# Kernel tuning notes

Hardware: AMD Instinct MI355X
Metric: run time of the kernel (lower is better)

## Reference

```python
import jax, jax.numpy as jnp
import numpy as np

B, S1, S2 = 16, 256, 512          # batch, vision len, text len
V_HID, T_HID = 1024, 768          # v_hidden_size, hidden_size
BI_HID, H = 1024, 8               # bi_hidden_size, bi_num_attention_heads
D = BI_HID // H                   # attention_head_size = 128


def setup_inputs() -> dict:
    key = jax.random.key(0)
    ks = jax.random.split(key, 16)
    s = 0.02
    inp = {
        "input_tensor1": jax.random.normal(ks[0], (B, S1, V_HID), jnp.float32),
        "attention_mask1": jnp.zeros((B, 1, 1, S1), jnp.float32),
        "input_tensor2": jax.random.normal(ks[1], (B, S2, T_HID), jnp.float32),
        "attention_mask2": jnp.zeros((B, 1, 1, S2), jnp.float32),
        # vision-stream projections (query1/key1/value1): v_hidden -> all_head_size
        "Wq1": jax.random.normal(ks[2], (V_HID, BI_HID), jnp.float32) * s,
        "bq1": jnp.zeros((BI_HID,), jnp.float32),
        "Wk1": jax.random.normal(ks[3], (V_HID, BI_HID), jnp.float32) * s,
        "bk1": jnp.zeros((BI_HID,), jnp.float32),
        "Wv1": jax.random.normal(ks[4], (V_HID, BI_HID), jnp.float32) * s,
        "bv1": jnp.zeros((BI_HID,), jnp.float32),
        # text-stream projections (query2/key2/value2): hidden -> all_head_size
        "Wq2": jax.random.normal(ks[5], (T_HID, BI_HID), jnp.float32) * s,
        "bq2": jnp.zeros((BI_HID,), jnp.float32),
        "Wk2": jax.random.normal(ks[6], (T_HID, BI_HID), jnp.float32) * s,
        "bk2": jnp.zeros((BI_HID,), jnp.float32),
        "Wv2": jax.random.normal(ks[7], (T_HID, BI_HID), jnp.float32) * s,
        "bv2": jnp.zeros((BI_HID,), jnp.float32),
    }
    return inp


def _heads(x):
    # [B, S, H*D] -> [B, S, H, D]
    b, s, _ = x.shape
    return x.reshape(b, s, H, D)


def reference(input_tensor1, attention_mask1, input_tensor2, attention_mask2,
              Wq1, bq1, Wk1, bk1, Wv1, bv1,
              Wq2, bq2, Wk2, bk2, Wv2, bv2):
    scale = 1.0 / jnp.sqrt(jnp.asarray(D, input_tensor1.dtype))
    # stream 1 (vision) QKV
    q1 = _heads(input_tensor1 @ Wq1 + bq1)
    k1 = _heads(input_tensor1 @ Wk1 + bk1)
    v1 = _heads(input_tensor1 @ Wv1 + bv1)
    # stream 2 (text) QKV
    q2 = _heads(input_tensor2 @ Wq2 + bq2)
    k2 = _heads(input_tensor2 @ Wk2 + bk2)
    v2 = _heads(input_tensor2 @ Wv2 + bv2)

    # attention 1: text queries attend to vision keys/values  -> context1 [B,S2,BI_HID]
    scores1 = jnp.einsum('bqhd,bkhd->bhqk', q2, k1) * scale + attention_mask1
    probs1 = jax.nn.softmax(scores1, axis=-1)  # dropout prob = 0 (eval)
    context1 = jnp.einsum('bhqk,bkhd->bqhd', probs1, v1).reshape(B, S2, BI_HID)

    # attention 2: vision queries attend to text keys/values  -> context2 [B,S1,BI_HID]
    scores2 = jnp.einsum('bqhd,bkhd->bhqk', q1, k2) * scale + attention_mask2
    probs2 = jax.nn.softmax(scores2, axis=-1)
    context2 = jnp.einsum('bhqk,bkhd->bqhd', probs2, v2).reshape(B, S1, BI_HID)

    return (context1, context2)
```

## Files before the change

### kernel.cpp

```cpp
#include <hip/hip_runtime.h>


typedef _Float16 f16;
typedef unsigned int u32;
typedef f16  v8h __attribute__((ext_vector_type(8)));
typedef float v4f __attribute__((ext_vector_type(4)));

struct alignas(8) h4 { f16 x, y, z, w; };

#define GLL16(g, l) __builtin_amdgcn_global_load_lds(                          \
    (const __attribute__((address_space(1))) u32*)(g),                         \
    (__attribute__((address_space(3))) u32*)(l), 16, 0, 0)

#define MFMA16 __builtin_amdgcn_mfma_f32_16x16x32_f16

__global__ __launch_bounds__(256)
void cvt_in(const float* __restrict__ p1, long n1,
            const float* __restrict__ p2, long n2,
            f16* __restrict__ d1, f16* __restrict__ d2)
{
    long i = ((long)blockIdx.x * 256 + threadIdx.x) * 8;
    const float* s; f16* d;
    if (i < n1) { s = p1 + i; d = d1 + i; }
    else        { long j = i - n1; if (j >= n2) return; s = p2 + j; d = d2 + j; }
    float4 a = *(const float4*)s, b = *(const float4*)(s + 4);
    v8h o = {(f16)a.x, (f16)a.y, (f16)a.z, (f16)a.w,
             (f16)b.x, (f16)b.y, (f16)b.z, (f16)b.w};
    *(v8h*)d = o;
}

__global__ __launch_bounds__(256)
void cvt_wT(const float* __restrict__ w0, const float* __restrict__ w1,
            const float* __restrict__ w2, const float* __restrict__ w3,
            const float* __restrict__ w4, const float* __restrict__ w5,
            f16* __restrict__ o1, f16* __restrict__ o2)
{
    const int z = blockIdx.z;
    const int K = z < 3 ? 1024 : 768;
    const int bk = blockIdx.y * 64;
    if (bk >= K) return;
    const float* src = z == 0 ? w0 : z == 1 ? w1 : z == 2 ? w2
                     : z == 3 ? w3 : z == 4 ? w4 : w5;
    f16* dst = z < 3 ? o1 + (size_t)z * 1024 * 1024
                     : o2 + (size_t)(z - 3) * 1024 * 768;

    __shared__ float t[64][65];
    const int bn = blockIdx.x * 64;
    const int r0 = threadIdx.x >> 4, c4 = (threadIdx.x & 15) * 4;
#pragma unroll
    for (int rr = 0; rr < 64; rr += 16) {
        float4 v = *(const float4*)&src[(long)(bk + rr + r0) * 1024 + bn + c4];
        t[rr + r0][c4 + 0] = v.x; t[rr + r0][c4 + 1] = v.y;
        t[rr + r0][c4 + 2] = v.z; t[rr + r0][c4 + 3] = v.w;
    }
    __syncthreads();
#pragma unroll
    for (int rr = 0; rr < 64; rr += 16) {
        const int n = rr + r0;
        h4 o = {(f16)t[c4 + 0][n], (f16)t[c4 + 1][n],
                (f16)t[c4 + 2][n], (f16)t[c4 + 3][n]};
        *(h4*)&dst[(long)(bn + n) * K + bk + c4] = o;
    }
}

__global__ __launch_bounds__(256, 4)
void mm_proj(const f16* __restrict__ A2, const f16* __restrict__ B2,
             const float* __restrict__ bq2, const float* __restrict__ bk2,
             const float* __restrict__ bv2,
             f16* __restrict__ q2o, f16* __restrict__ k2o, f16* __restrict__ v2o,
             const f16* __restrict__ A1, const f16* __restrict__ B1,
             const float* __restrict__ bq1, const float* __restrict__ bk1,
             const float* __restrict__ bv1,
             f16* __restrict__ q1o, f16* __restrict__ k1o, f16* __restrict__ v1o)
{
    __shared__ f16 sh[16384];

    const int gid = blockIdx.x;
    const bool is2 = gid < 1536;
    const int id   = is2 ? gid : gid - 1536;
    const int K    = is2 ? 768 : 1024;
    const int S    = is2 ? 512 : 256;
    const int mdiv = is2 ? 8 : 4;
    const f16* A  = is2 ? A2 : A1;
    const f16* Bw = is2 ? B2 : B1;

    const int by = (id & 7) * mdiv + ((id >> 3) % mdiv);
    const int bx = id / (8 * mdiv);
    const int m0 = by * 128, n0 = bx * 128;

    const int tid = threadIdx.x, lane = tid & 63, w = tid >> 6;
    const int wm = w >> 1, wn = w & 1;
    const int fr = lane & 15, fq = lane >> 4;

    int aoff[4], boff[4];
#pragma unroll
    for (int t = 0; t < 4; ++t) {
        const int ra = wm * 64 + t * 16 + fr;
        aoff[t] = ra * 32 + (fq ^ ((ra >> 1) & 3)) * 8;
        const int rb = wn * 64 + t * 16 + fr;
        boff[t] = rb * 32 + (fq ^ ((rb >> 1) & 3)) * 8;
    }

    auto stage = [&](int k0, int p) {
        f16* Ad = sh + p * 4096;
        f16* Bd = sh + 8192 + p * 4096;
#pragma unroll
        for (int j = 0; j < 2; ++j) {
            const int c = j * 256 + tid, row = c >> 2;
            const int kl = (c & 3) ^ ((row >> 1) & 3);
            GLL16(A  + (long)(m0 + row) * K + k0 + kl * 8, Ad + c * 8);
            GLL16(Bw + (long)(n0 + row) * K + k0 + kl * 8, Bd + c * 8);
        }
    };

    v4f acc[4][4];
#pragma unroll
    for (int i = 0; i < 4; ++i)
#pragma unroll
        for (int j = 0; j < 4; ++j) acc[i][j] = (v4f){0.f, 0.f, 0.f, 0.f};

    stage(0, 0);
    const int NK = K >> 5;
    for (int kt = 0; kt < NK; ++kt) {
        __syncthreads();
        if (kt + 1 < NK) stage((kt + 1) << 5, (kt + 1) & 1);
        const f16* As = sh + (kt & 1) * 4096;
        const f16* Bs = sh + 8192 + (kt & 1) * 4096;
        v8h ah[4], bh[4];
#pragma unroll
        for (int t = 0; t < 4; ++t) ah[t] = *(const v8h*)&As[aoff[t]];
#pragma unroll
        for (int t = 0; t < 4; ++t) bh[t] = *(const v8h*)&Bs[boff[t]];
#pragma unroll
        for (int tmi = 0; tmi < 4; ++tmi)
#pragma unroll
            for (int tni = 0; tni < 4; ++tni)
                acc[tmi][tni] = MFMA16(ah[tmi], bh[tni], acc[tmi][tni], 0, 0, 0);
    }

    const int col = lane & 15, quad = lane >> 4;
    const int seg = n0 >> 10, nbase = n0 & 1023;
    f16* buf = sh;

    if (seg < 2) {
        const float* bias = seg == 0 ? (is2 ? bq2 : bq1) : (is2 ? bk2 : bk1);
        f16* Co = seg == 0 ? (is2 ? q2o : q1o) : (is2 ? k2o : k1o);
#pragma unroll
        for (int pass = 0; pass < 2; ++pass) {
            __syncthreads();
            if (wm == pass) {
#pragma unroll
                for (int tmi = 0; tmi < 4; ++tmi) {
                    const int ml = tmi * 16 + quad * 4;
#pragma unroll
                    for (int tni = 0; tni < 4; ++tni) {
                        const int nl = wn * 64 + tni * 16 + col;
                        const float bvl = bias[nbase + nl];
#pragma unroll
                        for (int i = 0; i < 4; ++i)
                            buf[(ml + i) * 136 + nl] = (f16)(acc[tmi][tni][i] + bvl);
                    }
                }
            }
            __syncthreads();
            const int rr = tid >> 2, cc = (tid & 3) * 32;
            const long gb = (long)(m0 + pass * 64 + rr) * 1024 + nbase + cc;
#pragma unroll
            for (int c = 0; c < 4; ++c)
                *(v8h*)&Co[gb + c * 8] = *(const v8h*)&buf[rr * 136 + cc + c * 8];
        }
    } else {
        const float* bias = is2 ? bv2 : bv1;
        f16* vo = is2 ? v2o : v1o;
        const int bb = m0 / S, s0 = m0 % S;
#pragma unroll
        for (int pass = 0; pass < 2; ++pass) {
            __syncthreads();
            if (wn == pass) {
#pragma unroll
                for (int tmi = 0; tmi < 4; ++tmi) {
                    const int ml = wm * 64 + tmi * 16 + quad * 4;
#pragma unroll
                    for (int tni = 0; tni < 4; ++tni) {
                        const int nl = tni * 16 + col;
                        const float bvl = bias[nbase + pass * 64 + nl];
                        h4 o = {(f16)(acc[tmi][tni][0] + bvl),
                                (f16)(acc[tmi][tni][1] + bvl),
                                (f16)(acc[tmi][tni][2] + bvl),
                                (f16)(acc[tmi][tni][3] + bvl)};
                        *(h4*)&buf[nl * 136 + ml] = o;
                    }
                }
            }
            __syncthreads();
            const int nn = tid >> 2, mm = (tid & 3) * 32;
            const long gb = ((long)bb * 1024 + nbase + pass * 64 + nn) * S + s0 + mm;
#pragma unroll
            for (int c = 0; c < 4; ++c)
                *(v8h*)&vo[gb + c * 8] = *(const v8h*)&buf[nn * 136 + mm + c * 8];
        }
    }
}

__global__ __launch_bounds__(256, 2)
void flash(const f16* __restrict__ q2, const f16* __restrict__ k1,
           const f16* __restrict__ v1, const float* __restrict__ m1,
           float* __restrict__ o1,
           const f16* __restrict__ q1, const f16* __restrict__ k2,
           const f16* __restrict__ v2, const float* __restrict__ m2,
           float* __restrict__ o2, float scale)
{
    constexpr int PSTR = 72;
    __shared__ f16 lds[16384 + 128 * PSTR];
    f16* KL = lds;
    f16* VL = lds + 8192;
    f16* PL = lds + 16384;

    const int gid = blockIdx.x;
    const bool ph2 = gid < 256;
    const int id = ph2 ? gid : gid - 256;
    const int Sq = ph2 ? 256 : 512, Sk = ph2 ? 512 : 256;
    const f16* qp = ph2 ? q1 : q2;
    const f16* kp = ph2 ? k2 : k1;
    const f16* vp = ph2 ? v2 : v1;
    const float* mask = ph2 ? m2 : m1;
    float* out = ph2 ? o2 : o1;

    const int zz = id & 127, yy = id >> 7;
    const int b = zz >> 3, hd = zz & 7;
    const int q0 = yy * 128;
    const int tid = threadIdx.x, lane = tid & 63, w = tid >> 6;
    const int col = lane & 15, quad = lane >> 4;

    v8h qf[2][4];
#pragma unroll
    for (int rt = 0; rt < 2; ++rt) {
        const long qr = ((long)b * Sq + q0 + w * 32 + rt * 16 + col) * 1024
                        + (long)hd * 128;
#pragma unroll
        for (int kf = 0; kf < 4; ++kf)
            qf[rt][kf] = *(const v8h*)(qp + qr + kf * 32 + quad * 8);
    }

    v8h ones;
#pragma unroll
    for (int i = 0; i < 8; ++i) ones[i] = (f16)1.0f;

    v4f O[2][8], Lc[2];
#pragma unroll
    for (int rt = 0; rt < 2; ++rt) {
#pragma unroll
        for (int nj = 0; nj < 8; ++nj) O[rt][nj] = (v4f){0.f, 0.f, 0.f, 0.f};
        Lc[rt] = (v4f){0.f, 0.f, 0.f, 0.f};
    }

    const long kbase = (long)b * Sk * 1024 + (long)hd * 128;
    const long vbase = ((long)b * 1024 + hd * 128) * (long)Sk;
    const int nk = Sk >> 6;

    float mv[4];
#pragma unroll
    for (int tn = 0; tn < 4; ++tn)
        mv[tn] = mask[(long)b * Sk + tn * 16 + col];

    for (int kt = 0; kt < nk; ++kt) {
        __syncthreads();
#pragma unroll
        for (int j = 0; j < 4; ++j) {
            const int c = j * 256 + tid, row = c >> 4, ch = (c & 15) ^ (row & 15);
            GLL16(kp + kbase + (long)(kt * 64 + row) * 1024 + ch * 8, KL + c * 8);
        }
#pragma unroll
        for (int j = 0; j < 4; ++j) {
            const int c = j * 256 + tid, row = c >> 3, ch = (c & 7) ^ (row & 7);
            GLL16(vp + vbase + (long)row * Sk + kt * 64 + ch * 8, VL + c * 8);
        }
        float mvn[4];
        if (kt + 1 < nk) {
#pragma unroll
            for (int tn = 0; tn < 4; ++tn)
                mvn[tn] = mask[(long)b * Sk + (kt + 1) * 64 + tn * 16 + col];
        }
        __syncthreads();

        v4f sa[2][4];
#pragma unroll
        for (int rt = 0; rt < 2; ++rt)
#pragma unroll
            for (int tn = 0; tn < 4; ++tn) sa[rt][tn] = (v4f){0.f, 0.f, 0.f, 0.f};
#pragma unroll
        for (int kf = 0; kf < 4; ++kf) {
            v8h bh[4];
#pragma unroll
            for (int tn = 0; tn < 4; ++tn) {
                const int row = tn * 16 + col;
                bh[tn] = *(const v8h*)&KL[row * 128 + ((kf * 4 + quad) ^ (row & 15)) * 8];
            }
#pragma unroll
            for (int rt = 0; rt < 2; ++rt)
#pragma unroll
                for (int tn = 0; tn < 4; ++tn)
                    sa[rt][tn] = MFMA16(qf[rt][kf], bh[tn], sa[rt][tn], 0, 0, 0);
        }

#pragma unroll
        for (int rt = 0; rt < 2; ++rt)
#pragma unroll
            for (int tn = 0; tn < 4; ++tn)
#pragma unroll
                for (int r = 0; r < 4; ++r) {
                    const float p = __expf(sa[rt][tn][r] * scale + mv[tn]);
                    PL[(w * 32 + rt * 16 + quad * 4 + r) * PSTR + tn * 16 + col]
                        = (f16)p;
                }

#pragma unroll
        for (int kf2 = 0; kf2 < 2; ++kf2) {
            v8h vb[8];
#pragma unroll
            for (int nj = 0; nj < 8; ++nj) {
                const int row = nj * 16 + col;
                vb[nj] = *(const v8h*)&VL[row * 64 + ((kf2 * 4 + quad) ^ (row & 7)) * 8];
            }
#pragma unroll
            for (int rt = 0; rt < 2; ++rt) {
                const v8h pa = *(const v8h*)&PL[(w * 32 + rt * 16 + col) * PSTR
                                                + kf2 * 32 + quad * 8];
#pragma unroll
                for (int nj = 0; nj < 8; ++nj)
                    O[rt][nj] = MFMA16(pa, vb[nj], O[rt][nj], 0, 0, 0);
                Lc[rt] = MFMA16(pa, ones, Lc[rt], 0, 0, 0);
            }
        }
#pragma unroll
        for (int tn = 0; tn < 4; ++tn) mv[tn] = mvn[tn];
    }

#pragma unroll
    for (int rt = 0; rt < 2; ++rt) {
        float inv[4];
#pragma unroll
        for (int r = 0; r < 4; ++r) inv[r] = 1.0f / Lc[rt][r];
        const long ob = ((long)b * Sq + q0 + w * 32 + rt * 16 + quad * 4) * 1024
                        + (long)hd * 128;
#pragma unroll
        for (int nj = 0; nj < 8; ++nj)
#pragma unroll
            for (int r = 0; r < 4; ++r)
                out[ob + (long)r * 1024 + nj * 16 + col] = O[rt][nj][r] * inv[r];
    }
}

extern "C" void kernel_launch(void* const* d_in, const int* in_sizes, int n_in,
                              void* d_out, int out_size, void* d_ws, size_t ws_size,
                              hipStream_t stream)
{
    const float* in1   = (const float*)d_in[0];
    const float* mask1 = (const float*)d_in[1];
    const float* in2   = (const float*)d_in[2];
    const float* mask2 = (const float*)d_in[3];
    const float* Wq1 = (const float*)d_in[4];  const float* bq1 = (const float*)d_in[5];
    const float* Wk1 = (const float*)d_in[6];  const float* bk1 = (const float*)d_in[7];
    const float* Wv1 = (const float*)d_in[8];  const float* bv1 = (const float*)d_in[9];
    const float* Wq2 = (const float*)d_in[10]; const float* bq2 = (const float*)d_in[11];
    const float* Wk2 = (const float*)d_in[12]; const float* bk2 = (const float*)d_in[13];
    const float* Wv2 = (const float*)d_in[14]; const float* bv2 = (const float*)d_in[15];

    constexpr int Bb = 16, S1 = 256, S2 = 512, VH = 1024, TH = 768;
    constexpr long M1 = (long)Bb * S1, M2 = (long)Bb * S2;
    const float scale = 0.088388347648318447f;

    f16* W = (f16*)d_ws;
    f16* i1  = W;
    f16* i2  = i1 + M1 * VH;
    f16* w1  = i2 + M2 * TH;
    f16* w2  = w1 + (long)3072 * VH;
    f16* q1  = w2 + (long)3072 * TH;
    f16* k1  = q1 + M1 * 1024;
    f16* v1t = k1 + M1 * 1024;
    f16* q2  = v1t + M1 * 1024;
    f16* k2  = q2 + M2 * 1024;
    f16* v2t = k2 + M2 * 1024;
    float* out = (float*)d_out;

    cvt_in<<<dim3(5120), 256, 0, stream>>>(in1, M1 * VH, in2, M2 * TH, i1, i2);
    cvt_wT<<<dim3(16, 16, 6), 256, 0, stream>>>(Wq1, Wk1, Wv1, Wq2, Wk2, Wv2, w1, w2);

    mm_proj<<<dim3(2304), 256, 0, stream>>>(
        i2, w2, bq2, bk2, bv2, q2, k2, v2t,
        i1, w1, bq1, bk1, bv1, q1, k1, v1t);

    flash<<<dim3(768), 256, 0, stream>>>(
        q2, k1, v1t, mask1, out,
        q1, k2, v2t, mask2, out + M2 * 1024, scale);
}
```

Baseline: 251.3 us.

## Rewrite QKV projection GEMM with 256x256 tiles, 8 waves and deep async pipeline

Rewrites the projection GEMM to use 256x256 output tiles computed by 512 threads (8 waves), with a 64-wide K step, XOR-swizzled LDS layout, and a multi-stage global_load_lds pipeline using explicit vmcnt waits, barriers and setprio around MFMA clusters. Block ids are remapped across 8 groups (XCD-aware ordering), and the grid shrinks from 2304 to 576 blocks. The aim is more data reuse per LDS load and better overlap of loads with MFMA work. In exchange it needs 128KB of LDS and many accumulator registers, and with 576 blocks the tail and occupancy balance on the device may suffer.

```diff
diff --git a/kernel.cpp b/kernel.cpp
--- a/kernel.cpp
+++ b/kernel.cpp
@@ -63,141 +63,175 @@
     }
 }
 
-__global__ __launch_bounds__(256, 4)
-void mm_proj(const f16* __restrict__ A2, const f16* __restrict__ B2,
+__global__ __launch_bounds__(512, 2)
+void mm_proj(const f16* __restrict__ A1, const f16* __restrict__ B1,
+             const float* __restrict__ bq1, const float* __restrict__ bk1,
+             const float* __restrict__ bv1,
+             f16* __restrict__ q1o, f16* __restrict__ k1o, f16* __restrict__ v1o,
+             const f16* __restrict__ A2, const f16* __restrict__ B2,
              const float* __restrict__ bq2, const float* __restrict__ bk2,
              const float* __restrict__ bv2,
-             f16* __restrict__ q2o, f16* __restrict__ k2o, f16* __restrict__ v2o,
-             const f16* __restrict__ A1, const f16* __restrict__ B1,
-             const float* __restrict__ bq1, const float* __restrict__ bk1,
-             const float* __restrict__ bv1,
-             f16* __restrict__ q1o, f16* __restrict__ k1o, f16* __restrict__ v1o)
+             f16* __restrict__ q2o, f16* __restrict__ k2o, f16* __restrict__ v2o)
 {
-    __shared__ f16 sh[16384];
-
-    const int gid = blockIdx.x;
-    const bool is2 = gid < 1536;
-    const int id   = is2 ? gid : gid - 1536;
-    const int K    = is2 ? 768 : 1024;
-    const int S    = is2 ? 512 : 256;
-    const int mdiv = is2 ? 8 : 4;
-    const f16* A  = is2 ? A2 : A1;
-    const f16* Bw = is2 ? B2 : B1;
-
-    const int by = (id & 7) * mdiv + ((id >> 3) % mdiv);
-    const int bx = id / (8 * mdiv);
-    const int m0 = by * 128, n0 = bx * 128;
+    __shared__ f16 sh[65536];
+
+    const int orig = blockIdx.x;
+    const int lg = (orig & 7) * 72 + (orig >> 3);
+    const bool is1 = lg < 192;
+    const int id = is1 ? lg : lg - 192;
+    const int K  = is1 ? 1024 : 768;
+    const int by = is1 ? (id & 15) : (id & 31);
+    const int bx = is1 ? (id >> 4) : (id >> 5);
+    const int m0 = by << 8, n0 = bx << 8;
+    const f16* A  = is1 ? A1 : A2;
+    const f16* Bw = is1 ? B1 : B2;
 
     const int tid = threadIdx.x, lane = tid & 63, w = tid >> 6;
-    const int wm = w >> 1, wn = w & 1;
-    const int fr = lane & 15, fq = lane >> 4;
-
-    int aoff[4], boff[4];
-#pragma unroll
-    for (int t = 0; t < 4; ++t) {
-        const int ra = wm * 64 + t * 16 + fr;
-        aoff[t] = ra * 32 + (fq ^ ((ra >> 1) & 3)) * 8;
-        const int rb = wn * 64 + t * 16 + fr;
-        boff[t] = rb * 32 + (fq ^ ((rb >> 1) & 3)) * 8;
-    }
-
-    auto stage = [&](int k0, int p) {
-        f16* Ad = sh + p * 4096;
-        f16* Bd = sh + 8192 + p * 4096;
-#pragma unroll
-        for (int j = 0; j < 2; ++j) {
-            const int c = j * 256 + tid, row = c >> 2;
-            const int kl = (c & 3) ^ ((row >> 1) & 3);
-            GLL16(A  + (long)(m0 + row) * K + k0 + kl * 8, Ad + c * 8);
-            GLL16(Bw + (long)(n0 + row) * K + k0 + kl * 8, Bd + c * 8);
+    const int wm = w >> 2, wn = w & 3;
+    const int fr = lane & 15, quad = lane >> 4;
+    const int r7 = fr & 7;
+    const int NKT = K >> 6;
+
+    auto stage = [&](int h) {
+        const int kt = h >> 2, j = h & 3;
+        f16* dst = sh + (kt & 1) * 32768 + (j < 2 ? 16384 : 0) + (j & 1) * 8192;
+        const f16* src = (j < 2)
+            ? Bw + (long)(n0 + (j & 1) * 128) * K
+            : A  + (long)(m0 + (j & 1) * 128) * K;
+        const long kc = (long)kt << 6;
+#pragma unroll
+        for (int i = 0; i < 2; ++i) {
+            const int s = i * 512 + tid;
+            const int rh = s >> 3, ch = s & 7;
+            GLL16(src + (long)rh * K + kc + ((ch ^ (rh & 7)) << 3), dst + s * 8);
         }
     };
 
-    v4f acc[4][4];
-#pragma unroll
-    for (int i = 0; i < 4; ++i)
+    v4f acc[8][4];
+#pragma unroll
+    for (int i = 0; i < 8; ++i)
 #pragma unroll
         for (int j = 0; j < 4; ++j) acc[i][j] = (v4f){0.f, 0.f, 0.f, 0.f};
 
-    stage(0, 0);
-    const int NK = K >> 5;
-    for (int kt = 0; kt < NK; ++kt) {
-        __syncthreads();
-        if (kt + 1 < NK) stage((kt + 1) << 5, (kt + 1) & 1);
-        const f16* As = sh + (kt & 1) * 4096;
-        const f16* Bs = sh + 8192 + (kt & 1) * 4096;
-        v8h ah[4], bh[4];
-#pragma unroll
-        for (int t = 0; t < 4; ++t) ah[t] = *(const v8h*)&As[aoff[t]];
-#pragma unroll
-        for (int t = 0; t < 4; ++t) bh[t] = *(const v8h*)&Bs[boff[t]];
-#pragma unroll
-        for (int tmi = 0; tmi < 4; ++tmi)
-#pragma unroll
-            for (int tni = 0; tni < 4; ++tni)
-                acc[tmi][tni] = MFMA16(ah[tmi], bh[tni], acc[tmi][tni], 0, 0, 0);
-    }
-
-    const int col = lane & 15, quad = lane >> 4;
+#pragma unroll
+    for (int h = 0; h < 7; ++h) stage(h);
+    asm volatile("s_waitcnt vmcnt(6)" ::: "memory");
+    __builtin_amdgcn_s_barrier();
+
+    for (int k = 0; k < NKT; ++k) {
+        const f16* Ab = sh + (k & 1) * 32768 + wm * 8192;
+        const f16* Bb = sh + (k & 1) * 32768 + 16384 + (wn >> 1) * 8192;
+        const int brh = (wn & 1) * 64;
+        v8h bfrag[4][2];
+#pragma unroll
+        for (int q = 0; q < 4; ++q) {
+            if (q == 0) {
+#pragma unroll
+                for (int n = 0; n < 4; ++n) {
+                    const int rh = brh + n * 16 + fr;
+                    const f16* p = Bb + rh * 64;
+#pragma unroll
+                    for (int kf = 0; kf < 2; ++kf)
+                        bfrag[n][kf] = *(const v8h*)&p[(((kf << 2) + quad) ^ r7) << 3];
+                }
+            }
+            v8h af[2][2];
+#pragma unroll
+            for (int mf = 0; mf < 2; ++mf) {
+                const int rh = q * 32 + mf * 16 + fr;
+                const f16* p = Ab + rh * 64;
+#pragma unroll
+                for (int kf = 0; kf < 2; ++kf)
+                    af[mf][kf] = *(const v8h*)&p[(((kf << 2) + quad) ^ r7) << 3];
+            }
+            const int h = (k << 2) + 7 + q;
+            if (h < (NKT << 2)) stage(h);
+            __builtin_amdgcn_s_barrier();
+            asm volatile("s_waitcnt lgkmcnt(0)" ::: "memory");
+            __builtin_amdgcn_sched_barrier(0);
+            __builtin_amdgcn_s_setprio(1);
+#pragma unroll
+            for (int kf = 0; kf < 2; ++kf)
+#pragma unroll
+                for (int mf = 0; mf < 2; ++mf)
+#pragma unroll
+                    for (int n = 0; n < 4; ++n)
+                        acc[q * 2 + mf][n] = MFMA16(af[mf][kf], bfrag[n][kf],
+                                                    acc[q * 2 + mf][n], 0, 0, 0);
+            __builtin_amdgcn_s_setprio(0);
+            if (q == 3) {
+                if (k + 2 < NKT) asm volatile("s_waitcnt vmcnt(6)" ::: "memory");
+                else             asm volatile("s_waitcnt vmcnt(0)" ::: "memory");
+            }
+            __builtin_amdgcn_s_barrier();
+        }
+    }
+
+    const int col = fr;
     const int seg = n0 >> 10, nbase = n0 & 1023;
     f16* buf = sh;
 
     if (seg < 2) {
-        const float* bias = seg == 0 ? (is2 ? bq2 : bq1) : (is2 ? bk2 : bk1);
-        f16* Co = seg == 0 ? (is2 ? q2o : q1o) : (is2 ? k2o : k1o);
+        const float* bias = seg == 0 ? (is1 ? bq1 : bq2) : (is1 ? bk1 : bk2);
+        f16* Co = seg == 0 ? (is1 ? q1o : q2o) : (is1 ? k1o : k2o);
+        float bl[4];
+#pragma unroll
+        for (int n = 0; n < 4; ++n) bl[n] = bias[nbase + wn * 64 + n * 16 + col];
 #pragma unroll
         for (int pass = 0; pass < 2; ++pass) {
             __syncthreads();
             if (wm == pass) {
 #pragma unroll
-                for (int tmi = 0; tmi < 4; ++tmi) {
-                    const int ml = tmi * 16 + quad * 4;
-#pragma unroll
-                    for (int tni = 0; tni < 4; ++tni) {
-                        const int nl = wn * 64 + tni * 16 + col;
-                        const float bvl = bias[nbase + nl];
-#pragma unroll
-                        for (int i = 0; i < 4; ++i)
-                            buf[(ml + i) * 136 + nl] = (f16)(acc[tmi][tni][i] + bvl);
+                for (int mi = 0; mi < 8; ++mi) {
+                    const int ml = mi * 16 + quad * 4;
+#pragma unroll
+                    for (int n = 0; n < 4; ++n) {
+                        const int nl = wn * 64 + n * 16 + col;
+#pragma unroll
+                        for (int r = 0; r < 4; ++r)
+                            buf[(ml + r) * 264 + nl] = (f16)(acc[mi][n][r] + bl[n]);
                     }
                 }
             }
             __syncthreads();
-            const int rr = tid >> 2, cc = (tid & 3) * 32;
-            const long gb = (long)(m0 + pass * 64 + rr) * 1024 + nbase + cc;
-#pragma unroll
-            for (int c = 0; c < 4; ++c)
-                *(v8h*)&Co[gb + c * 8] = *(const v8h*)&buf[rr * 136 + cc + c * 8];
+            const int rr = tid >> 2, cc = (tid & 3) * 64;
+            const long gb = (long)(m0 + pass * 128 + rr) * 1024 + nbase + cc;
+#pragma unroll
+            for (int c = 0; c < 8; ++c)
+                *(v8h*)&Co[gb + c * 8] = *(const v8h*)&buf[rr * 264 + cc + c * 8];
         }
     } else {
-        const float* bias = is2 ? bv2 : bv1;
-        f16* vo = is2 ? v2o : v1o;
+        const float* bias = is1 ? bv1 : bv2;
+        f16* vo = is1 ? v1o : v2o;
+        const int S = is1 ? 256 : 512;
         const int bb = m0 / S, s0 = m0 % S;
+        float bl[4];
+#pragma unroll
+        for (int n = 0; n < 4; ++n) bl[n] = bias[nbase + wn * 64 + n * 16 + col];
 #pragma unroll
         for (int pass = 0; pass < 2; ++pass) {
             __syncthreads();
-            if (wn == pass) {
-#pragma unroll
-                for (int tmi = 0; tmi < 4; ++tmi) {
-                    const int ml = wm * 64 + tmi * 16 + quad * 4;
-#pragma unroll
-                    for (int tni = 0; tni < 4; ++tni) {
-                        const int nl = tni * 16 + col;
-                        const float bvl = bias[nbase + pass * 64 + nl];
-                        h4 o = {(f16)(acc[tmi][tni][0] + bvl),
-                                (f16)(acc[tmi][tni][1] + bvl),
-                                (f16)(acc[tmi][tni][2] + bvl),
-                                (f16)(acc[tmi][tni][3] + bvl)};
-                        *(h4*)&buf[nl * 136 + ml] = o;
+            if ((wn >> 1) == pass) {
+#pragma unroll
+                for (int mi = 0; mi < 8; ++mi) {
+                    const int ml = wm * 128 + mi * 16 + quad * 4;
+#pragma unroll
+                    for (int n = 0; n < 4; ++n) {
+                        const int nl = (wn & 1) * 64 + n * 16 + col;
+                        h4 o = {(f16)(acc[mi][n][0] + bl[n]),
+                                (f16)(acc[mi][n][1] + bl[n]),
+                                (f16)(acc[mi][n][2] + bl[n]),
+                                (f16)(acc[mi][n][3] + bl[n])};
+                        *(h4*)&buf[nl * 264 + ml] = o;
                     }
                 }
             }
             __syncthreads();
-            const int nn = tid >> 2, mm = (tid & 3) * 32;
-            const long gb = ((long)bb * 1024 + nbase + pass * 64 + nn) * S + s0 + mm;
-#pragma unroll
-            for (int c = 0; c < 4; ++c)
-                *(v8h*)&vo[gb + c * 8] = *(const v8h*)&buf[nn * 136 + mm + c * 8];
+            const int nn = tid >> 2, mm = (tid & 3) * 64;
+            const long gb = ((long)bb * 1024 + nbase + pass * 128 + nn) * S + s0 + mm;
+#pragma unroll
+            for (int c = 0; c < 8; ++c)
+                *(v8h*)&vo[gb + c * 8] = *(const v8h*)&buf[nn * 264 + mm + c * 8];
         }
     }
 }
@@ -386,9 +420,9 @@
     cvt_in<<<dim3(5120), 256, 0, stream>>>(in1, M1 * VH, in2, M2 * TH, i1, i2);
     cvt_wT<<<dim3(16, 16, 6), 256, 0, stream>>>(Wq1, Wk1, Wv1, Wq2, Wk2, Wv2, w1, w2);
 
-    mm_proj<<<dim3(2304), 256, 0, stream>>>(
-        i2, w2, bq2, bk2, bv2, q2, k2, v2t,
-        i1, w1, bq1, bk1, bv1, q1, k1, v1t);
+    mm_proj<<<dim3(576), 512, 0, stream>>>(
+        i1, w1, bq1, bk1, bv1, q1, k1, v1t,
+        i2, w2, bq2, bk2, bv2, q2, k2, v2t);
 
     flash<<<dim3(768), 256, 0, stream>>>(
         q2, k1, v1t, mask1, out,
```

After: 283.6 us. 1.13x slower.
